# Performance work log

Hardware: AMD Instinct MI355X
Metric: run time of the kernel (lower is better)

Reference implementation:

```python
import jax, jax.numpy as jnp
import numpy as np

HIDDEN = 1152
HEADS = 16
HEAD_DIM = HIDDEN // HEADS  # 72
SCALE = HEAD_DIM ** -0.5


def setup_inputs() -> dict:
    key = jax.random.key(0)
    ks = jax.random.split(key, 9)
    B, S = 16, 729
    init = lambda k, shape: jax.random.normal(k, shape, dtype=jnp.float32) * (shape[0] ** -0.5)
    return {
        "hidden_states": jax.random.normal(ks[0], (B, S, HIDDEN), dtype=jnp.float32),
        "Wq": init(ks[1], (HIDDEN, HIDDEN)), "bq": jnp.zeros((HIDDEN,), jnp.float32),
        "Wk": init(ks[2], (HIDDEN, HIDDEN)), "bk": jnp.zeros((HIDDEN,), jnp.float32),
        "Wv": init(ks[3], (HIDDEN, HIDDEN)), "bv": jnp.zeros((HIDDEN,), jnp.float32),
        "Wo": init(ks[4], (HIDDEN, HIDDEN)), "bo": jnp.zeros((HIDDEN,), jnp.float32),
    }


def reference(hidden_states, Wq, bq, Wk, bk, Wv, bv, Wo, bo):
    B, S, D = hidden_states.shape
    # QKV projections, split heads: [B, S, H, Dh]
    q = (hidden_states @ Wq + bq).reshape(B, S, HEADS, HEAD_DIM)
    k = (hidden_states @ Wk + bk).reshape(B, S, HEADS, HEAD_DIM)
    v = (hidden_states @ Wv + bv).reshape(B, S, HEADS, HEAD_DIM)
    # Scores: [B, H, S, S]
    scores = jnp.einsum("bqhd,bkhd->bhqk", q, k) * jnp.asarray(SCALE, q.dtype)
    # Softmax computed in float32 (as in the original layer), cast back
    attn = jax.nn.softmax(scores.astype(jnp.float32), axis=-1).astype(q.dtype)
    # Weighted values: [B, S, H, Dh] -> [B, S, D]
    out = jnp.einsum("bhqk,bkhd->bqhd", attn, v).reshape(B, S, D)
    return out @ Wo + bo
```

## Files before the change

kernel.cpp:

```cpp
#include <hip/hip_runtime.h>
#include <hip/hip_bf16.h>

#define HD    1152
#define NHD   16
#define DH    72
#define DHP   80
#define NB    16
#define SEQ   729
#define SP    736
#define MTOT  (NB*SEQ)
#define MPAD  11776
#define VROWS 96
#define QSCALE (0.117851130197757930f * 1.4426950408889634f)

typedef __attribute__((ext_vector_type(8))) short short8;
typedef __attribute__((ext_vector_type(4))) float f32x4;
typedef __attribute__((ext_vector_type(16))) float f32x16;
typedef __attribute__((ext_vector_type(4))) unsigned u32x4;
typedef unsigned short us;

__device__ __forceinline__ us f2bf(float x){
  unsigned u = __float_as_uint(x);
  u += 0x7FFFu + ((u >> 16) & 1u);
  return (us)(u >> 16);
}

__device__ __forceinline__ unsigned cvtpk_bf16(float lo, float hi){
  unsigned r;
  asm("v_cvt_pk_bf16_f32 %0, %1, %2" : "=v"(r) : "v"(lo), "v"(hi));
  return r;
}

#define GLD16(g, s) __builtin_amdgcn_global_load_lds( \
    (const __attribute__((address_space(1))) void*)(g), \
    (__attribute__((address_space(3))) void*)(s), 16, 0, 0)

#define OFF_HSB   ((size_t)0)
#define OFF_WQKV  ((size_t)27131904)
#define OFF_WO    ((size_t)35094528)
#define OFF_Q     ((size_t)37748736)
#define OFF_K     ((size_t)67608576)
#define OFF_V     ((size_t)97755136)
#define WS_END    ((size_t)133931008)

#define CVT_BLOCKS 13122
__global__ void prep_kernel(const float* __restrict__ hs, us* __restrict__ hsb,
                            const float* __restrict__ Wq, const float* __restrict__ Wk,
                            const float* __restrict__ Wv, const float* __restrict__ Wo,
                            us* __restrict__ wqkvT, us* __restrict__ woT){
  __shared__ float t[32][33];
  const int b = blockIdx.x, tid = threadIdx.x;
  if (b < CVT_BLOCKS){
    int i = b*256 + tid;
    float4 v = ((const float4*)hs)[i];
    ushort4 o;
    o.x = f2bf(v.x); o.y = f2bf(v.y); o.z = f2bf(v.z); o.w = f2bf(v.w);
    ((ushort4*)hsb)[i] = o;
    return;
  }
  const int bb = b - CVT_BLOCKS;
  const int sel = bb / 1296, cell = bb % 1296;
  const int k0 = (cell/36)*32, n0 = (cell%36)*32;
  const float* W = (sel==0)?Wq:(sel==1)?Wk:(sel==2)?Wv:Wo;
  us* outT = (sel<3) ? (wqkvT + (size_t)sel*HD*HD) : woT;
  const int tx = tid & 31, ty = tid >> 5;
  #pragma unroll
  for (int j=0;j<32;j+=8) t[ty+j][tx] = W[(size_t)(k0+ty+j)*HD + n0 + tx];
  __syncthreads();
  #pragma unroll
  for (int j=0;j<32;j+=8) outT[(size_t)(n0+ty+j)*HD + k0 + tx] = f2bf(t[tx][ty+j]);
}

template<int MODE>
__global__ __launch_bounds__(512, 4) void gemm_kernel(
    const us* __restrict__ A, const us* __restrict__ BT,
    const float* __restrict__ bias_q, const float* __restrict__ bias_k,
    const float* __restrict__ bias_v,
    float* __restrict__ outF,
    us* __restrict__ Qp, us* __restrict__ Kp, us* __restrict__ Vt)
{
  constexpr int TILES_N = (MODE==1) ? 27 : 9;
  constexpr int NPAIRS  = 46;
  constexpr int NPHYS   = NPAIRS*TILES_N;
  constexpr int TCW     = 9;
  constexpr int NT = HD/32;

  int p;
  {
    int orig = blockIdx.x;
    constexpr int q = NPHYS >> 3, r = NPHYS & 7;
    int xcd = orig & 7, idx = orig >> 3;
    p = (xcd < r ? xcd*(q+1) : r*(q+1) + (xcd-r)*q) + idx;
  }
  const int tid = threadIdx.x, w = tid>>6, l = tid&63;
  const int g  = w>>2;
  const int wl = w&3;
  const int lr = l&15, lg = l>>4;
  const int wm = wl>>1, wn = wl&1;

  const int tc   = p / (NPAIRS*TCW);
  const int rem  = p - tc*(NPAIRS*TCW);
  const int tmp_ = rem / TCW;
  const int tnq  = rem - tmp_*TCW;
  const int tm = tmp_*2 + g;
  const int tn = tc*TCW + tnq;

  __shared__ __align__(16) us As[2][2][4096];
  __shared__ __align__(16) us Bs[2][4096];

  const int srow = wl*32 + (l>>2);
  const int scol = (l&3)*8;
  const us* gA = A  + (size_t)(tm*128 + srow)*HD + scol;
  const us* gB = BT + (size_t)(tn*128 + srow)*HD + scol;

#define STAGEP(kb, buf) do { \
    GLD16(gA + (kb),          &As[g][buf][wl*1024]); \
    GLD16(gA + (kb) + 16*HD,  &As[g][buf][wl*1024 + 512]); \
    if (g == 0){ \
      GLD16(gB + (kb),          &Bs[buf][wl*1024]); \
      GLD16(gB + (kb) + 16*HD,  &Bs[buf][wl*1024 + 512]); \
    } \
  } while(0)

  f32x4 acc[4][4];
  #pragma unroll
  for (int i=0;i<4;i++)
    #pragma unroll
    for (int j=0;j<4;j++) acc[i][j] = (f32x4){0.f,0.f,0.f,0.f};

  STAGEP(0, 0);
  STAGEP(32, 1);

  for (int kt = 0; kt < NT-1; kt++){
    const int cur = kt & 1;
    if (g == 0) asm volatile("s_waitcnt vmcnt(4)" ::: "memory");
    else        asm volatile("s_waitcnt vmcnt(2)" ::: "memory");
    __builtin_amdgcn_sched_barrier(0);
    __builtin_amdgcn_s_barrier();
    __builtin_amdgcn_sched_barrier(0);

    short8 af[4], bfr[4];
    #pragma unroll
    for (int mi=0;mi<4;mi++) af[mi]  = *(const short8*)(&As[g][cur][(wm*64 + mi*16 + lr)*32 + lg*8]);
    #pragma unroll
    for (int ni=0;ni<4;ni++) bfr[ni] = *(const short8*)(&Bs[cur][(wn*64 + ni*16 + lr)*32 + lg*8]);

    asm volatile("s_waitcnt lgkmcnt(0)" ::: "memory");
    __builtin_amdgcn_sched_barrier(0);
    __builtin_amdgcn_s_barrier();
    __builtin_amdgcn_sched_barrier(0);

    if (kt + 2 < NT) STAGEP((kt+2)*32, cur);

    __builtin_amdgcn_s_setprio(1);
    #pragma unroll
    for (int mi=0;mi<4;mi++)
      #pragma unroll
      for (int ni=0;ni<4;ni++)
        acc[mi][ni] = __builtin_amdgcn_mfma_f32_16x16x32_bf16(af[mi], bfr[ni], acc[mi][ni], 0, 0, 0);
    __builtin_amdgcn_s_setprio(0);
  }
  {
    constexpr int cur = (NT-1) & 1;
    asm volatile("s_waitcnt vmcnt(0)" ::: "memory");
    __builtin_amdgcn_sched_barrier(0);
    __builtin_amdgcn_s_barrier();
    __builtin_amdgcn_sched_barrier(0);
    short8 af[4], bfr[4];
    #pragma unroll
    for (int mi=0;mi<4;mi++) af[mi]  = *(const short8*)(&As[g][cur][(wm*64 + mi*16 + lr)*32 + lg*8]);
    #pragma unroll
    for (int ni=0;ni<4;ni++) bfr[ni] = *(const short8*)(&Bs[cur][(wn*64 + ni*16 + lr)*32 + lg*8]);
    #pragma unroll
    for (int mi=0;mi<4;mi++)
      #pragma unroll
      for (int ni=0;ni<4;ni++)
        acc[mi][ni] = __builtin_amdgcn_mfma_f32_16x16x32_bf16(af[mi], bfr[ni], acc[mi][ni], 0, 0, 0);
  }
#undef STAGEP

  if (MODE == 0){
    #pragma unroll
    for (int mi=0;mi<4;mi++){
      #pragma unroll
      for (int j=0;j<4;j++){
        int m = tm*128 + wm*64 + mi*16 + lg*4 + j;
        if (m < MTOT){
          #pragma unroll
          for (int ni=0;ni<4;ni++){
            int n = tn*128 + wn*64 + ni*16 + lr;
            outF[(size_t)m*HD + n] = acc[mi][ni][j] + bias_q[n];
          }
        }
      }
    }
  } else {
    asm volatile("s_waitcnt lgkmcnt(0)" ::: "memory");
    __builtin_amdgcn_sched_barrier(0);
    __builtin_amdgcn_s_barrier();
    __builtin_amdgcn_sched_barrier(0);

    if (tn >= 18){
      float* scr = (float*)(&As[0][0][0]) + w*(16*17);
      #pragma unroll
      for (int mi=0;mi<4;mi++){
        int m = tm*128 + wm*64 + mi*16 + lr;
        int b = m / SEQ;
        int s = m - b*SEQ;
        bool ok = (m < MTOT);
        #pragma unroll
        for (int ni=0;ni<4;ni++){
          #pragma unroll
          for (int j=0;j<4;j++) scr[(lg*4+j)*17 + lr] = acc[mi][ni][j];
          asm volatile("s_waitcnt lgkmcnt(0)" ::: "memory");
          float tv[4];
          #pragma unroll
          for (int j=0;j<4;j++) tv[j] = scr[lr*17 + lg*4 + j];
          asm volatile("s_waitcnt lgkmcnt(0)" ::: "memory");
          if (ok){
            #pragma unroll
            for (int j=0;j<4;j++){
              int n = tn*128 + wn*64 + ni*16 + lg*4 + j;
              int c = n - 2*HD;
              int h = c / DH;
              int d = c - h*DH;
              int bh = b*NHD + h;
              Vt[(size_t)bh*(VROWS*SP) + (size_t)d*SP + s] = f2bf(tv[j] + bias_v[c]);
            }
          }
        }
      }
    } else {
      const bool isQ = (tn < 9);
      const int nbase = isQ ? 0 : HD;
      const float* bias = isQ ? bias_q : bias_k;
      #pragma unroll
      for (int mi=0;mi<4;mi++){
        #pragma unroll
        for (int j=0;j<4;j++){
          int m = tm*128 + wm*64 + mi*16 + lg*4 + j;
          if (m >= MTOT) continue;
          int b = m / SEQ;
          int s = m - b*SEQ;
          #pragma unroll
          for (int ni=0;ni<4;ni++){
            int n = tn*128 + wn*64 + ni*16 + lr;
            int c = n - nbase;
            int h = c / DH;
            int d = c - h*DH;
            int bh = b*NHD + h;
            float v = acc[mi][ni][j] + bias[c];
            if (isQ){
              Qp[(size_t)bh*(SEQ*DHP) + (size_t)s*DHP + d] = f2bf(v*QSCALE);
              if (d < 8)
                Qp[(size_t)bh*(SEQ*DHP) + (size_t)s*DHP + 72 + d] = 0;
            } else {
              Kp[(size_t)bh*(SP*DHP) + (size_t)s*DHP + d] = f2bf(v);
            }
          }
        }
      }
    }
  }
}

__device__ __forceinline__ void pv_subtile(const f32x16 s, const us* __restrict__ vcol,
                                           int hi, f32x16 (&o)[3]){
  unsigned A[4], B[4], xA[4], xB[4];
  #pragma unroll
  for (int g=0; g<4; g++){
    A[g]  = cvtpk_bf16(s[4*g+0], s[4*g+1]);
    B[g]  = cvtpk_bf16(s[4*g+2], s[4*g+3]);
    xA[g] = (unsigned)__shfl_xor((int)A[g], 32);
    xB[g] = (unsigned)__shfl_xor((int)B[g], 32);
  }
  __builtin_amdgcn_s_setprio(1);
  #pragma unroll
  for (int ks=0; ks<2; ks++){
    unsigned w0 = hi ? xA[2*ks+1] : A[2*ks];
    unsigned w1 = hi ? xB[2*ks+1] : B[2*ks];
    unsigned w2 = hi ? A[2*ks+1]  : xA[2*ks];
    unsigned w3 = hi ? B[2*ks+1]  : xB[2*ks];
    u32x4 pw = {w0, w1, w2, w3};
    short8 pa = __builtin_bit_cast(short8, pw);
    #pragma unroll
    for (int dt=0; dt<3; dt++){
      short8 vf = *(const short8*)(vcol + (size_t)(dt*32)*SP + ks*16 + hi*8);
      o[dt] = __builtin_amdgcn_mfma_f32_32x32x16_bf16(pa, vf, o[dt], 0, 0, 0);
    }
  }
  __builtin_amdgcn_s_setprio(0);
}

__global__ __launch_bounds__(256) void attn_kernel(
    const us* __restrict__ Qp, const us* __restrict__ Kp,
    const us* __restrict__ Vt, us* __restrict__ ctx)
{
  const int blk = blockIdx.x;
  const int xcd = blk & 7, ii = blk >> 3;
  const int bh  = xcd*32 + ii/6;
  const int qt6 = ii % 6;
  const int tid = threadIdx.x, w = tid>>6, l = tid&63;
  const int lane = l & 31, hi = l >> 5;

  const int qbase = (qt6*4 + w)*32;
  if (qbase >= SEQ) return;

  const us* Qb = Qp + (size_t)bh*(SEQ*DHP);
  const us* Kb = Kp + (size_t)bh*(SP*DHP);
  const us* Vb = Vt + (size_t)bh*(VROWS*SP);

  int qr = qbase + lane; if (qr > SEQ-1) qr = SEQ-1;
  short8 qf[5];
  #pragma unroll
  for (int c=0;c<5;c++) qf[c] = *(const short8*)(Qb + (size_t)qr*DHP + c*16 + hi*8);

  f32x16 o[3];
  #pragma unroll
  for (int dt=0; dt<3; dt++)
    #pragma unroll
    for (int r=0;r<16;r++) o[dt][r] = 0.f;

  float lsum = 0.f;

  for (int kt=0; kt<12; kt++){
    const int kb = kt*64;
    f32x16 s0, s1;
    #pragma unroll
    for (int r=0;r<16;r++){ s0[r]=0.f; s1[r]=0.f; }

    const us* krow0 = Kb + (size_t)(kb + lane)*DHP + hi*8;
    __builtin_amdgcn_s_setprio(1);
    #pragma unroll
    for (int c=0;c<5;c++){
      short8 kf = *(const short8*)(krow0 + c*16);
      s0 = __builtin_amdgcn_mfma_f32_32x32x16_bf16(kf, qf[c], s0, 0, 0, 0);
    }
    __builtin_amdgcn_s_setprio(0);
    if (kt < 11){
      const us* krow1 = krow0 + 32*DHP;
      __builtin_amdgcn_s_setprio(1);
      #pragma unroll
      for (int c=0;c<5;c++){
        short8 kf = *(const short8*)(krow1 + c*16);
        s1 = __builtin_amdgcn_mfma_f32_32x32x16_bf16(kf, qf[c], s1, 0, 0, 0);
      }
      __builtin_amdgcn_s_setprio(0);
    } else {
      #pragma unroll
      for (int r=0;r<16;r++){
        const int base = 704 + (r&3) + 8*(r>>2);
        s0[r] = (base + 4*hi >= SEQ) ? -1e30f : s0[r];
        s1[r] = -1e30f;
      }
    }

    #pragma unroll
    for (int r=0;r<16;r++) s0[r] = exp2f(s0[r]);
    #pragma unroll
    for (int r=0;r<16;r++) s1[r] = exp2f(s1[r]);

    {
      float t[8];
      #pragma unroll
      for (int r=0;r<8;r++) t[r] = (s0[r] + s0[r+8]) + (s1[r] + s1[r+8]);
      #pragma unroll
      for (int r=0;r<4;r++) t[r] = t[r] + t[r+4];
      lsum += (t[0]+t[1]) + (t[2]+t[3]);
    }

    const us* vcol = Vb + (size_t)lane*SP + kb;
    pv_subtile(s0, vcol, hi, o);
    if (kt < 11) pv_subtile(s1, vcol + 32, hi, o);
  }

  lsum += __shfl_xor(lsum, 32);
  float linv = 1.0f / lsum;
  const int b = bh >> 4, h = bh & 15;
  #pragma unroll
  for (int r=0;r<16;r++){
    const int qloc = (r&3) + 8*(r>>2) + 4*hi;
    float lv = __shfl(linv, qloc);
    int q = qbase + qloc;
    if (q < SEQ){
      us* crow = ctx + ((size_t)(b*SEQ + q))*HD + h*DH;
      #pragma unroll
      for (int dt=0; dt<3; dt++){
        int d = dt*32 + lane;
        if (d < DH) crow[d] = f2bf(o[dt][r] * lv);
      }
    }
  }
}

extern "C" void kernel_launch(void* const* d_in, const int* in_sizes, int n_in,
                              void* d_out, int out_size, void* d_ws, size_t ws_size,
                              hipStream_t stream) {
  const float* hs = (const float*)d_in[0];
  const float* Wq = (const float*)d_in[1]; const float* bq = (const float*)d_in[2];
  const float* Wk = (const float*)d_in[3]; const float* bk = (const float*)d_in[4];
  const float* Wv = (const float*)d_in[5]; const float* bv = (const float*)d_in[6];
  const float* Wo = (const float*)d_in[7]; const float* bo = (const float*)d_in[8];
  float* out = (float*)d_out;
  char* ws = (char*)d_ws;
  if (ws_size < WS_END) return;

  us* hsb   = (us*)(ws + OFF_HSB);
  us* wqkvT = (us*)(ws + OFF_WQKV);
  us* woT   = (us*)(ws + OFF_WO);
  us* Qp    = (us*)(ws + OFF_Q);
  us* Kp    = (us*)(ws + OFF_K);
  us* Vt    = (us*)(ws + OFF_V);
  us* ctx   = hsb;

  prep_kernel<<<CVT_BLOCKS + 4*1296, 256, 0, stream>>>(hs, hsb, Wq, Wk, Wv, Wo,
                                                       wqkvT, woT);

  gemm_kernel<1><<<46*27, 512, 0, stream>>>(hsb, wqkvT, bq, bk, bv,
                                            nullptr, Qp, Kp, Vt);

  attn_kernel<<<1536, 256, 0, stream>>>(Qp, Kp, Vt, ctx);

  gemm_kernel<0><<<46*9, 512, 0, stream>>>(ctx, woT, bo, nullptr, nullptr,
                                           out, nullptr, nullptr, nullptr);
}
```

Measured before the change: 319.6 us.

## Stage K/V tiles into LDS with double-buffered async loads shared across waves

Attention now cooperatively loads each 64-key K tile and V tile into shared memory with direct global-to-LDS loads, double-buffered two tiles ahead. All four waves then read K/V fragments from LDS instead of each fetching them from global memory. The aim is to cut redundant global/L2 traffic and overlap loads with MFMA work. It adds block barriers and hand-tuned vmcnt waits, and removes the early exit for idle waves so they join the barriers, which increases synchronization cost and adds correctness risk.

```diff
diff --git a/kernel.cpp b/kernel.cpp
--- a/kernel.cpp
+++ b/kernel.cpp
@@ -264,8 +264,8 @@
   }
 }
 
-__device__ __forceinline__ void pv_subtile(const f32x16 s, const us* __restrict__ vcol,
-                                           int hi, f32x16 (&o)[3]){
+__device__ __forceinline__ void pv_subtile(const f32x16 s, const us* __restrict__ vb,
+                                           int hi, int lane, int sh, f32x16 (&o)[3]){
   unsigned A[4], B[4], xA[4], xB[4];
   #pragma unroll
   for (int g=0; g<4; g++){
@@ -285,7 +285,7 @@
     short8 pa = __builtin_bit_cast(short8, pw);
     #pragma unroll
     for (int dt=0; dt<3; dt++){
-      short8 vf = *(const short8*)(vcol + (size_t)(dt*32)*SP + ks*16 + hi*8);
+      short8 vf = *(const short8*)(vb + ((2*ks + hi + 4*sh)*96 + lane + dt*32)*8);
       o[dt] = __builtin_amdgcn_mfma_f32_32x32x16_bf16(pa, vf, o[dt], 0, 0, 0);
     }
   }
@@ -304,17 +304,41 @@
   const int lane = l & 31, hi = l >> 5;
 
   const int qbase = (qt6*4 + w)*32;
-  if (qbase >= SEQ) return;
 
   const us* Qb = Qp + (size_t)bh*(SEQ*DHP);
   const us* Kb = Kp + (size_t)bh*(SP*DHP);
   const us* Vb = Vt + (size_t)bh*(VROWS*SP);
 
+  __shared__ __align__(16) us lds[2][11264];
+
   int qr = qbase + lane; if (qr > SEQ-1) qr = SEQ-1;
   short8 qf[5];
   #pragma unroll
   for (int c=0;c<5;c++) qf[c] = *(const short8*)(Qb + (size_t)qr*DHP + c*16 + hi*8);
 
+  const int kr_c = (l < 32) ? l : 31;
+  int vu[3], vrow[3];
+  #pragma unroll
+  for (int j=0;j<3;j++){ int slot = (w+4*j)*64 + l; vu[j] = slot/96; vrow[j] = slot - vu[j]*96; }
+
+#define STAGE_KV(kt_, buf_) do { \
+    const int kb_ = (kt_)*64; \
+    const int kr_ = ((kt_) == 11) ? kr_c : l; \
+    _Pragma("unroll") \
+    for (int j_=0;j_<3;j_++){ \
+      int u_ = w + 4*j_; \
+      if (u_ < 10) \
+        GLD16(Kb + (size_t)(kb_ + kr_)*DHP + u_*8, &lds[buf_][u_*512]); \
+    } \
+    _Pragma("unroll") \
+    for (int j_=0;j_<3;j_++){ \
+      int i_ = w + 4*j_; \
+      int col_ = kb_ + vu[j_]*8; \
+      if (col_ > SP-8) col_ = SP-8; \
+      GLD16(Vb + (size_t)vrow[j_]*SP + col_, &lds[buf_][5120 + i_*512]); \
+    } \
+  } while(0)
+
   f32x16 o[3];
   #pragma unroll
   for (int dt=0; dt<3; dt++)
@@ -323,26 +347,40 @@
 
   float lsum = 0.f;
 
+  STAGE_KV(0, 0);
+  STAGE_KV(1, 1);
+
   for (int kt=0; kt<12; kt++){
-    const int kb = kt*64;
+    const int cur = kt & 1;
+    if (kt < 11){
+      if (w < 2) asm volatile("s_waitcnt vmcnt(6)" ::: "memory");
+      else       asm volatile("s_waitcnt vmcnt(5)" ::: "memory");
+    } else {
+      asm volatile("s_waitcnt vmcnt(0)" ::: "memory");
+    }
+    __builtin_amdgcn_sched_barrier(0);
+    __builtin_amdgcn_s_barrier();
+    __builtin_amdgcn_sched_barrier(0);
+
+    const us* kbase = &lds[cur][0];
+    const us* vbase = &lds[cur][5120];
+
     f32x16 s0, s1;
     #pragma unroll
     for (int r=0;r<16;r++){ s0[r]=0.f; s1[r]=0.f; }
 
-    const us* krow0 = Kb + (size_t)(kb + lane)*DHP + hi*8;
     __builtin_amdgcn_s_setprio(1);
     #pragma unroll
     for (int c=0;c<5;c++){
-      short8 kf = *(const short8*)(krow0 + c*16);
+      short8 kf = *(const short8*)(kbase + ((2*c+hi)*64 + lane)*8);
       s0 = __builtin_amdgcn_mfma_f32_32x32x16_bf16(kf, qf[c], s0, 0, 0, 0);
     }
     __builtin_amdgcn_s_setprio(0);
     if (kt < 11){
-      const us* krow1 = krow0 + 32*DHP;
       __builtin_amdgcn_s_setprio(1);
       #pragma unroll
       for (int c=0;c<5;c++){
-        short8 kf = *(const short8*)(krow1 + c*16);
+        short8 kf = *(const short8*)(kbase + ((2*c+hi)*64 + lane + 32)*8);
         s1 = __builtin_amdgcn_mfma_f32_32x32x16_bf16(kf, qf[c], s1, 0, 0, 0);
       }
       __builtin_amdgcn_s_setprio(0);
@@ -369,10 +407,17 @@
       lsum += (t[0]+t[1]) + (t[2]+t[3]);
     }
 
-    const us* vcol = Vb + (size_t)lane*SP + kb;
-    pv_subtile(s0, vcol, hi, o);
-    if (kt < 11) pv_subtile(s1, vcol + 32, hi, o);
-  }
+    pv_subtile(s0, vbase, hi, lane, 0, o);
+    if (kt < 11) pv_subtile(s1, vbase, hi, lane, 1, o);
+
+    asm volatile("s_waitcnt lgkmcnt(0)" ::: "memory");
+    __builtin_amdgcn_sched_barrier(0);
+    __builtin_amdgcn_s_barrier();
+    __builtin_amdgcn_sched_barrier(0);
+
+    if (kt + 2 < 12) STAGE_KV(kt+2, cur);
+  }
+#undef STAGE_KV
 
   lsum += __shfl_xor(lsum, 32);
   float linv = 1.0f / lsum;
```

New measurement: 284.3 us (median of 2 runs). 1.12x faster.
